# Optimization experiments

Hardware: AMD Instinct MI355X
Metric: run time of the kernel (lower is better)

The kernel has to match this reference:

```python
import jax, jax.numpy as jnp
import numpy as np

B = 16384
IN = 512
H = 512

def setup_inputs() -> dict:
    key = jax.random.key(0)
    k1, k2, k3, k4, k5, k6 = jax.random.split(key, 6)
    s_in = 1.0 / np.sqrt(IN + H)
    return {
        "x": jax.random.normal(k1, (B, IN), dtype=jnp.float32),
        "h": jax.random.normal(k2, (B, H), dtype=jnp.float32),
        # lin_in: (IN+H) -> 2H ; stored as [in_features, out_features]
        "W_in": jax.random.uniform(k3, (IN + H, 2 * H), minval=-s_in, maxval=s_in, dtype=jnp.float32),
        "b_in": jax.random.uniform(k4, (2 * H,), minval=-s_in, maxval=s_in, dtype=jnp.float32),
        # lin_out: (IN+H) -> H
        "W_out": jax.random.uniform(k5, (IN + H, H), minval=-s_in, maxval=s_in, dtype=jnp.float32),
        "b_out": jax.random.uniform(k6, (H,), minval=-s_in, maxval=s_in, dtype=jnp.float32),
    }

def reference(x, h, W_in, b_in, W_out, b_out):
    xh = jnp.concatenate([x, h], axis=1)              # [B, IN+H]
    lin = xh @ W_in + b_in                             # [B, 2H]
    learn_pre, forget_pre = jnp.split(lin, 2, axis=1)  # each [B, H]
    learn = jnp.tanh(learn_pre)
    forget_mult = jax.nn.sigmoid(forget_pre)
    h_new = forget_mult * h + (1.0 - forget_mult) * learn
    xh2 = jnp.concatenate([x, h_new], axis=1)          # [B, IN+H]
    out = jnp.tanh(xh2 @ W_out + b_out)                # [B, H]
    return (out, h_new)
```

## Files before the change

### kernel.cpp

```cpp
#include <hip/hip_runtime.h>
#include <cstdint>

typedef unsigned short ushort_t;
typedef __attribute__((ext_vector_type(4))) float f32x4;
typedef __attribute__((ext_vector_type(8))) __bf16 bf16x8;
typedef __attribute__((ext_vector_type(8))) unsigned short ushort8;

#define NB 16384
#define DK 1024

#define MFMA16(a, b, c) __builtin_amdgcn_mfma_f32_16x16x32_bf16(a, b, c, 0, 0, 0)

__device__ __forceinline__ unsigned short f2b(float f) {
    unsigned u = __builtin_bit_cast(unsigned, f);
    unsigned r = u + 0x7fffu + ((u >> 16) & 1u);
    return (unsigned short)(r >> 16);
}
__device__ __forceinline__ float b2f(ushort_t b) {
    unsigned u = ((unsigned)b) << 16;
    return __builtin_bit_cast(float, u);
}
__device__ __forceinline__ float fast_sigmoid(float x) {
    return __fdividef(1.0f, 1.0f + __expf(-x));
}
__device__ __forceinline__ float fast_tanh(float x) {
    return __fdividef(2.0f, 1.0f + __expf(-2.0f * x)) - 1.0f;
}

__device__ __forceinline__ void gll16(const void* g, void* lds) {
    __builtin_amdgcn_global_load_lds(
        (__attribute__((address_space(1))) unsigned int*)(uintptr_t)g,
        (__attribute__((address_space(3))) unsigned int*)(unsigned int)(uintptr_t)lds,
        16, 0, 0);
}


__global__ __launch_bounds__(256) void k_cvt(const float* __restrict__ x,
                                             const float* __restrict__ h,
                                             ushort_t* __restrict__ XB,
                                             ushort_t* __restrict__ HB) {
    int b = blockIdx.x;
    const float* s;
    ushort_t* d;
    if (b < 4096) { s = x; d = XB; } else { s = h; d = HB; b -= 4096; }
    size_t g = (size_t)b * 256 + threadIdx.x;
    const float* p = s + g * 8;
    f32x4 f0 = *(const f32x4*)p;
    f32x4 f1 = *(const f32x4*)(p + 4);
    ushort8 o;
#pragma unroll
    for (int j = 0; j < 4; ++j) { o[j] = f2b(f0[j]); o[j + 4] = f2b(f1[j]); }
    *(ushort8*)(d + g * 8) = o;
}

__global__ __launch_bounds__(256) void k_transpose_w(const float* __restrict__ Wi,
                                                     const float* __restrict__ Wo,
                                                     ushort_t* __restrict__ WTI,
                                                     ushort_t* __restrict__ WTO) {
    const int z = blockIdx.z;
    if (z == 1 && blockIdx.x >= 16) return;
    const float* W = (z == 0) ? Wi : Wo;
    ushort_t* Wt = (z == 0) ? WTI : WTO;
    const int ncols = (z == 0) ? 1024 : 512;
    __shared__ float tile[32][33];
    int n0 = blockIdx.x * 32, k0 = blockIdx.y * 32;
    int tx = threadIdx.x & 31, ty = threadIdx.x >> 5;
#pragma unroll
    for (int i = 0; i < 32; i += 8)
        tile[ty + i][tx] = W[(size_t)(k0 + ty + i) * ncols + n0 + tx];
    __syncthreads();
#pragma unroll
    for (int i = 0; i < 32; i += 8)
        Wt[(size_t)(n0 + ty + i) * DK + k0 + tx] = f2b(tile[tx][ty + i]);
}

__global__ __launch_bounds__(256, 4) void k_gemm1(
    const ushort_t* __restrict__ XB, const ushort_t* __restrict__ HB,
    const ushort_t* __restrict__ WT, const float* __restrict__ b_in,
    float* __restrict__ hnew, ushort_t* __restrict__ HN) {
    __shared__ ushort_t As[2][128 * 32];
    __shared__ ushort_t Bs[2][2][64 * 32];

    const int wg = blockIdx.x;
    const int xcd = wg & 7, kk_ = wg >> 3;
    const int m0 = ((xcd << 4) | (kk_ & 15)) * 128;
    const int n0 = (kk_ >> 4) * 64;

    const int t = threadIdx.x;
    const int lane = t & 63;
    const int wave = t >> 6;
    const int wm = wave >> 1, wn = wave & 1;

    f32x4 accL[4][2] = {};
    f32x4 accF[4][2] = {};

    const int srow = t >> 2;
    const int skel = (t & 3) * 8;
    const size_t arow = (size_t)(m0 + srow) * 512;
    const ushort_t* gBL = WT + (size_t)(n0 + srow) * DK + skel;
    const ushort_t* gBF = WT + (size_t)(n0 + 512 + srow) * DK + skel;

    auto stage = [&](int it, int buf) {
        const int kt = it * 32;
        const ushort_t* abase =
            (kt < 512) ? (XB + arow + kt + skel) : (HB + arow + (kt - 512) + skel);
        ushort_t* a = &As[buf][t * 8];
        gll16(abase, a);
        gll16(abase + 64 * 512, a + 64 * 32);
        gll16(gBL + kt, &Bs[buf][0][t * 8]);
        gll16(gBF + kt, &Bs[buf][1][t * 8]);
    };

    const int fr = lane & 15;
    const int kq = (lane >> 4) * 8;

    stage(0, 0);
    int cur = 0;
    for (int it = 0; it < 32; ++it) {
        asm volatile("s_waitcnt vmcnt(0)" ::: "memory");
        __syncthreads();
        if (it + 1 < 32) stage(it + 1, cur ^ 1);

        bf16x8 av[4], blv[2], bfv[2];
#pragma unroll
        for (int i = 0; i < 4; ++i)
            av[i] = *(const bf16x8*)(&As[cur][(wm * 64 + i * 16 + fr) * 32 + kq]);
#pragma unroll
        for (int j = 0; j < 2; ++j) {
            blv[j] = *(const bf16x8*)(&Bs[cur][0][(wn * 32 + j * 16 + fr) * 32 + kq]);
            bfv[j] = *(const bf16x8*)(&Bs[cur][1][(wn * 32 + j * 16 + fr) * 32 + kq]);
        }
#pragma unroll
        for (int i = 0; i < 4; ++i)
#pragma unroll
            for (int j = 0; j < 2; ++j) {
                accL[i][j] = MFMA16(av[i], blv[j], accL[i][j]);
                accF[i][j] = MFMA16(av[i], bfv[j], accF[i][j]);
            }
        cur ^= 1;
    }

    const int fq = lane >> 4;
#pragma unroll
    for (int i = 0; i < 4; ++i)
#pragma unroll
        for (int j = 0; j < 2; ++j) {
            const int c = n0 + wn * 32 + j * 16 + fr;
            const float bl = b_in[c];
            const float bf = b_in[c + 512];
#pragma unroll
            for (int rr = 0; rr < 4; ++rr) {
                const int row = m0 + wm * 64 + i * 16 + fq * 4 + rr;
                float lp = accL[i][j][rr] + bl;
                float fp = accF[i][j][rr] + bf;
                float hv = b2f(HB[(size_t)row * 512 + c]);
                float fm = fast_sigmoid(fp);
                float lr = fast_tanh(lp);
                float hn = lr + fm * (hv - lr);
                hnew[(size_t)row * 512 + c] = hn;
                HN[(size_t)row * 512 + c] = f2b(hn);
            }
        }
}

__global__ __launch_bounds__(256, 3) void k_gemm2(
    const ushort_t* __restrict__ XB, const ushort_t* __restrict__ HN,
    const ushort_t* __restrict__ WT, const float* __restrict__ b_out,
    float* __restrict__ out) {
    __shared__ ushort_t As[2][128 * 32];
    __shared__ ushort_t Bs[2][128 * 32];

    const int wg = blockIdx.x;
    const int xcd = wg & 7, kk_ = wg >> 3;
    const int m0 = ((xcd << 4) | (kk_ & 15)) * 128;
    const int n0 = (kk_ >> 4) * 128;

    const int t = threadIdx.x;
    const int lane = t & 63;
    const int wave = t >> 6;
    const int wm = wave >> 1, wn = wave & 1;

    f32x4 acc[4][4] = {};

    const int srow = t >> 2;
    const int skel = (t & 3) * 8;
    const size_t arow = (size_t)(m0 + srow) * 512;
    const ushort_t* gB = WT + (size_t)(n0 + srow) * DK + skel;

    auto stage = [&](int it, int buf) {
        const int kt = it * 32;
        const ushort_t* abase =
            (kt < 512) ? (XB + arow + kt + skel) : (HN + arow + (kt - 512) + skel);
        ushort_t* a = &As[buf][t * 8];
        ushort_t* b = &Bs[buf][t * 8];
        gll16(abase, a);
        gll16(abase + 64 * 512, a + 64 * 32);
        gll16(gB + kt, b);
        gll16(gB + kt + 64 * DK, b + 64 * 32);
    };

    const int fr = lane & 15;
    const int kq = (lane >> 4) * 8;

    stage(0, 0);
    int cur = 0;
    for (int it = 0; it < 32; ++it) {
        asm volatile("s_waitcnt vmcnt(0)" ::: "memory");
        __syncthreads();
        if (it + 1 < 32) stage(it + 1, cur ^ 1);

        bf16x8 av[4], bv[4];
#pragma unroll
        for (int i = 0; i < 4; ++i) {
            av[i] = *(const bf16x8*)(&As[cur][(wm * 64 + i * 16 + fr) * 32 + kq]);
            bv[i] = *(const bf16x8*)(&Bs[cur][(wn * 64 + i * 16 + fr) * 32 + kq]);
        }
#pragma unroll
        for (int i = 0; i < 4; ++i)
#pragma unroll
            for (int j = 0; j < 4; ++j)
                acc[i][j] = MFMA16(av[i], bv[j], acc[i][j]);
        cur ^= 1;
    }

    const int fq = lane >> 4;
#pragma unroll
    for (int i = 0; i < 4; ++i)
#pragma unroll
        for (int j = 0; j < 4; ++j) {
            const int c = n0 + wn * 64 + j * 16 + fr;
            const float bo = b_out[c];
#pragma unroll
            for (int rr = 0; rr < 4; ++rr) {
                const int row = m0 + wm * 64 + i * 16 + fq * 4 + rr;
                out[(size_t)row * 512 + c] = fast_tanh(acc[i][j][rr] + bo);
            }
        }
}

extern "C" void kernel_launch(void* const* d_in, const int* in_sizes, int n_in,
                              void* d_out, int out_size, void* d_ws, size_t ws_size,
                              hipStream_t stream) {
    const float* x = (const float*)d_in[0];
    const float* h = (const float*)d_in[1];
    const float* W_in = (const float*)d_in[2];
    const float* b_in = (const float*)d_in[3];
    const float* W_out = (const float*)d_in[4];
    const float* b_out = (const float*)d_in[5];

    float* out = (float*)d_out;
    float* hnew = out + (size_t)NB * 512;

    ushort_t* XB = (ushort_t*)d_ws;
    ushort_t* HB = XB + (size_t)NB * 512;
    ushort_t* HN = HB + (size_t)NB * 512;
    ushort_t* WTI = HN + (size_t)NB * 512;
    ushort_t* WTO = WTI + (size_t)1024 * 1024;

    k_cvt<<<8192, 256, 0, stream>>>(x, h, XB, HB);
    k_transpose_w<<<dim3(32, 32, 2), 256, 0, stream>>>(W_in, W_out, WTI, WTO);
    k_gemm1<<<1024, 256, 0, stream>>>(XB, HB, WTI, b_in, hnew, HN);
    k_gemm2<<<512, 256, 0, stream>>>(XB, HN, WTO, b_out, out);
}
```

Measured before the change: 94.35 us.

## Double K-tile depth to 64, add MFMA priority hints, prefetch h early

Both GEMM kernels now stage 64-wide K tiles, halving the number of barrier/wait iterations and doubling the work per sync, with launch bounds lowered to 2 blocks per CU to fit the larger LDS. MFMA bursts are wrapped in s_setprio to favor the matrix issue over other waves. gemm1 also loads the h values needed in the epilogue partway through the main loop so their latency overlaps with compute. The larger LDS footprint lowers occupancy, which may hide less latency. LDS row stride becomes 64 elements, which can cause bank conflicts on the fragment reads.

```diff
diff --git a/kernel.cpp b/kernel.cpp
--- a/kernel.cpp
+++ b/kernel.cpp
@@ -74,17 +74,17 @@
         Wt[(size_t)(n0 + ty + i) * DK + k0 + tx] = f2b(tile[tx][ty + i]);
 }
 
-__global__ __launch_bounds__(256, 4) void k_gemm1(
+__global__ __launch_bounds__(256, 2) void k_gemm1(
     const ushort_t* __restrict__ XB, const ushort_t* __restrict__ HB,
     const ushort_t* __restrict__ WT, const float* __restrict__ b_in,
     float* __restrict__ hnew, ushort_t* __restrict__ HN) {
-    __shared__ ushort_t As[2][128 * 32];
-    __shared__ ushort_t Bs[2][2][64 * 32];
+    __shared__ ushort_t As[2][128 * 64];
+    __shared__ ushort_t Bs[2][2][64 * 64];
 
     const int wg = blockIdx.x;
-    const int xcd = wg & 7, kk_ = wg >> 3;
-    const int m0 = ((xcd << 4) | (kk_ & 15)) * 128;
-    const int n0 = (kk_ >> 4) * 64;
+    const int xcd = wg & 7, q = wg >> 3;
+    const int m0 = ((xcd << 4) | (q & 15)) * 128;
+    const int n0 = (q >> 4) * 64;
 
     const int t = threadIdx.x;
     const int lane = t & 63;
@@ -94,53 +94,73 @@
     f32x4 accL[4][2] = {};
     f32x4 accF[4][2] = {};
 
-    const int srow = t >> 2;
-    const int skel = (t & 3) * 8;
-    const size_t arow = (size_t)(m0 + srow) * 512;
+    const int srow = t >> 3;
+    const int skel = (t & 7) * 8;
     const ushort_t* gBL = WT + (size_t)(n0 + srow) * DK + skel;
     const ushort_t* gBF = WT + (size_t)(n0 + 512 + srow) * DK + skel;
 
     auto stage = [&](int it, int buf) {
-        const int kt = it * 32;
-        const ushort_t* abase =
-            (kt < 512) ? (XB + arow + kt + skel) : (HB + arow + (kt - 512) + skel);
+        const int kt = it * 64;
+        const ushort_t* ab = (kt < 512)
+            ? (XB + (size_t)(m0 + srow) * 512 + kt + skel)
+            : (HB + (size_t)(m0 + srow) * 512 + (kt - 512) + skel);
         ushort_t* a = &As[buf][t * 8];
-        gll16(abase, a);
-        gll16(abase + 64 * 512, a + 64 * 32);
-        gll16(gBL + kt, &Bs[buf][0][t * 8]);
-        gll16(gBF + kt, &Bs[buf][1][t * 8]);
+#pragma unroll
+        for (int r = 0; r < 4; ++r)
+            gll16(ab + (size_t)(32 * r) * 512, a + 2048 * r);
+#pragma unroll
+        for (int r = 0; r < 2; ++r) {
+            gll16(gBL + kt + (size_t)(32 * r) * DK, &Bs[buf][0][t * 8 + 2048 * r]);
+            gll16(gBF + kt + (size_t)(32 * r) * DK, &Bs[buf][1][t * 8 + 2048 * r]);
+        }
     };
 
     const int fr = lane & 15;
-    const int kq = (lane >> 4) * 8;
+    const int fq = lane >> 4;
+    const int kq = fq * 8;
+
+    ushort_t hv_us[4][2][4];
 
     stage(0, 0);
-    int cur = 0;
-    for (int it = 0; it < 32; ++it) {
+    for (int it = 0; it < 16; ++it) {
         asm volatile("s_waitcnt vmcnt(0)" ::: "memory");
         __syncthreads();
-        if (it + 1 < 32) stage(it + 1, cur ^ 1);
-
-        bf16x8 av[4], blv[2], bfv[2];
-#pragma unroll
-        for (int i = 0; i < 4; ++i)
-            av[i] = *(const bf16x8*)(&As[cur][(wm * 64 + i * 16 + fr) * 32 + kq]);
-#pragma unroll
-        for (int j = 0; j < 2; ++j) {
-            blv[j] = *(const bf16x8*)(&Bs[cur][0][(wn * 32 + j * 16 + fr) * 32 + kq]);
-            bfv[j] = *(const bf16x8*)(&Bs[cur][1][(wn * 32 + j * 16 + fr) * 32 + kq]);
-        }
-#pragma unroll
-        for (int i = 0; i < 4; ++i)
+        if (it + 1 < 16) stage(it + 1, (it + 1) & 1);
+        if (it == 11) {
+#pragma unroll
+            for (int i = 0; i < 4; ++i)
+#pragma unroll
+                for (int j = 0; j < 2; ++j)
+#pragma unroll
+                    for (int rr = 0; rr < 4; ++rr)
+                        hv_us[i][j][rr] =
+                            HB[(size_t)(m0 + wm * 64 + i * 16 + fq * 4 + rr) * 512 +
+                               n0 + wn * 32 + j * 16 + fr];
+        }
+        const int cur = it & 1;
+#pragma unroll
+        for (int kk = 0; kk < 2; ++kk) {
+            bf16x8 av[4], blv[2], bfv[2];
+#pragma unroll
+            for (int i = 0; i < 4; ++i)
+                av[i] = *(const bf16x8*)(&As[cur][(wm * 64 + i * 16 + fr) * 64 + kk * 32 + kq]);
 #pragma unroll
             for (int j = 0; j < 2; ++j) {
-                accL[i][j] = MFMA16(av[i], blv[j], accL[i][j]);
-                accF[i][j] = MFMA16(av[i], bfv[j], accF[i][j]);
-            }
-        cur ^= 1;
+                blv[j] = *(const bf16x8*)(&Bs[cur][0][(wn * 32 + j * 16 + fr) * 64 + kk * 32 + kq]);
+                bfv[j] = *(const bf16x8*)(&Bs[cur][1][(wn * 32 + j * 16 + fr) * 64 + kk * 32 + kq]);
+            }
+            __builtin_amdgcn_s_setprio(1);
+#pragma unroll
+            for (int i = 0; i < 4; ++i)
+#pragma unroll
+                for (int j = 0; j < 2; ++j) {
+                    accL[i][j] = MFMA16(av[i], blv[j], accL[i][j]);
+                    accF[i][j] = MFMA16(av[i], bfv[j], accF[i][j]);
+                }
+            __builtin_amdgcn_s_setprio(0);
+        }
     }
 
-    const int fq = lane >> 4;
 #pragma unroll
     for (int i = 0; i < 4; ++i)
 #pragma unroll
@@ -153,7 +173,7 @@
                 const int row = m0 + wm * 64 + i * 16 + fq * 4 + rr;
                 float lp = accL[i][j][rr] + bl;
                 float fp = accF[i][j][rr] + bf;
-                float hv = b2f(HB[(size_t)row * 512 + c]);
+                float hv = b2f(hv_us[i][j][rr]);
                 float fm = fast_sigmoid(fp);
                 float lr = fast_tanh(lp);
                 float hn = lr + fm * (hv - lr);
@@ -163,17 +183,17 @@
         }
 }
 
-__global__ __launch_bounds__(256, 3) void k_gemm2(
+__global__ __launch_bounds__(256, 2) void k_gemm2(
     const ushort_t* __restrict__ XB, const ushort_t* __restrict__ HN,
     const ushort_t* __restrict__ WT, const float* __restrict__ b_out,
     float* __restrict__ out) {
-    __shared__ ushort_t As[2][128 * 32];
-    __shared__ ushort_t Bs[2][128 * 32];
+    __shared__ ushort_t As[2][128 * 64];
+    __shared__ ushort_t Bs[2][128 * 64];
 
     const int wg = blockIdx.x;
-    const int xcd = wg & 7, kk_ = wg >> 3;
-    const int m0 = ((xcd << 4) | (kk_ & 15)) * 128;
-    const int n0 = (kk_ >> 4) * 128;
+    const int xcd = wg & 7, q = wg >> 3;
+    const int m0 = ((xcd << 4) | (q & 15)) * 128;
+    const int n0 = (q >> 4) * 128;
 
     const int t = threadIdx.x;
     const int lane = t & 63;
@@ -182,48 +202,52 @@
 
     f32x4 acc[4][4] = {};
 
-    const int srow = t >> 2;
-    const int skel = (t & 3) * 8;
-    const size_t arow = (size_t)(m0 + srow) * 512;
+    const int srow = t >> 3;
+    const int skel = (t & 7) * 8;
     const ushort_t* gB = WT + (size_t)(n0 + srow) * DK + skel;
 
     auto stage = [&](int it, int buf) {
-        const int kt = it * 32;
-        const ushort_t* abase =
-            (kt < 512) ? (XB + arow + kt + skel) : (HN + arow + (kt - 512) + skel);
+        const int kt = it * 64;
+        const ushort_t* ab = (kt < 512)
+            ? (XB + (size_t)(m0 + srow) * 512 + kt + skel)
+            : (HN + (size_t)(m0 + srow) * 512 + (kt - 512) + skel);
         ushort_t* a = &As[buf][t * 8];
         ushort_t* b = &Bs[buf][t * 8];
-        gll16(abase, a);
-        gll16(abase + 64 * 512, a + 64 * 32);
-        gll16(gB + kt, b);
-        gll16(gB + kt + 64 * DK, b + 64 * 32);
+#pragma unroll
+        for (int r = 0; r < 4; ++r) {
+            gll16(ab + (size_t)(32 * r) * 512, a + 2048 * r);
+            gll16(gB + kt + (size_t)(32 * r) * DK, b + 2048 * r);
+        }
     };
 
     const int fr = lane & 15;
-    const int kq = (lane >> 4) * 8;
+    const int fq = lane >> 4;
+    const int kq = fq * 8;
 
     stage(0, 0);
-    int cur = 0;
-    for (int it = 0; it < 32; ++it) {
+    for (int it = 0; it < 16; ++it) {
         asm volatile("s_waitcnt vmcnt(0)" ::: "memory");
         __syncthreads();
-        if (it + 1 < 32) stage(it + 1, cur ^ 1);
-
-        bf16x8 av[4], bv[4];
-#pragma unroll
-        for (int i = 0; i < 4; ++i) {
-            av[i] = *(const bf16x8*)(&As[cur][(wm * 64 + i * 16 + fr) * 32 + kq]);
-            bv[i] = *(const bf16x8*)(&Bs[cur][(wn * 64 + i * 16 + fr) * 32 + kq]);
-        }
-#pragma unroll
-        for (int i = 0; i < 4; ++i)
-#pragma unroll
-            for (int j = 0; j < 4; ++j)
-                acc[i][j] = MFMA16(av[i], bv[j], acc[i][j]);
-        cur ^= 1;
+        if (it + 1 < 16) stage(it + 1, (it + 1) & 1);
+        const int cur = it & 1;
+#pragma unroll
+        for (int kk = 0; kk < 2; ++kk) {
+            bf16x8 av[4], bv[4];
+#pragma unroll
+            for (int i = 0; i < 4; ++i) {
+                av[i] = *(const bf16x8*)(&As[cur][(wm * 64 + i * 16 + fr) * 64 + kk * 32 + kq]);
+                bv[i] = *(const bf16x8*)(&Bs[cur][(wn * 64 + i * 16 + fr) * 64 + kk * 32 + kq]);
+            }
+            __builtin_amdgcn_s_setprio(1);
+#pragma unroll
+            for (int i = 0; i < 4; ++i)
+#pragma unroll
+                for (int j = 0; j < 4; ++j)
+                    acc[i][j] = MFMA16(av[i], bv[j], acc[i][j]);
+            __builtin_amdgcn_s_setprio(0);
+        }
     }
 
-    const int fq = lane >> 4;
 #pragma unroll
     for (int i = 0; i < 4; ++i)
 #pragma unroll
```

Result: no change. 95.87 us (+1.6%).
